# Kernel optimization log

Measured on AMD Instinct MI355X. Metric: run time of the kernel, lower is better.

## Reference

```python
import jax, jax.numpy as jnp
import numpy as np

H = 128          # hidden_dim
E = 1048576      # num edges
N = 262144       # num nodes
T = 4096         # num targets / subgraphs
NET = 8          # num_edge_types
SCALAR_DIM = 32  # max(H // 4, 8)
SHORT = 1.0      # short_time_scale
LONG = 24.0      # long_time_scale


def _ln(x):
    # F.layer_norm without affine params, eps=1e-5, biased variance
    m = jnp.mean(x, axis=-1, keepdims=True)
    v = jnp.var(x, axis=-1, keepdims=True)
    return (x - m) / jnp.sqrt(v + 1e-5)


def _seg_wmean(vals, gid, w, num_groups):
    # masked/weighted segment mean: mask is folded into w (zeros drop rows)
    num = jax.ops.segment_sum(vals * w[:, None], gid, num_segments=num_groups)
    den = jax.ops.segment_sum(w, gid, num_segments=num_groups)
    return num / jnp.maximum(den, 1e-6)[:, None]


def setup_inputs():
    key = jax.random.key(0)
    ks = jax.random.split(key, 14)
    node_repr = jax.random.normal(ks[0], (N, H), jnp.float32)
    edge_repr = jax.random.normal(ks[1], (E, H), jnp.float32)
    edge_src = jax.random.randint(ks[2], (E,), 0, N)
    edge_subgraph_id = jax.random.randint(ks[3], (E,), 0, T)
    node_subgraph_id = jax.random.randint(ks[4], (N,), 0, T)
    node_hop_depth = jax.random.randint(ks[5], (N,), 1, 4)
    rel_ids = jax.random.randint(ks[6], (E,), 0, 2 * NET)
    edge_relative_time = jax.random.uniform(ks[7], (E,), jnp.float32) * 48.0
    target_local_idx = jnp.arange(T, dtype=jnp.int32)
    base_dst = jax.random.randint(ks[8], (E,), 0, N)
    hit = jax.random.uniform(ks[9], (E,)) < 0.25
    edge_dst = jnp.where(hit, target_local_idx[edge_subgraph_id], base_dst)
    # scalar_proj: Linear(8, 32); fuse: Linear(8*H+32, 2*H) -> GELU -> Linear(2*H, H)
    W1 = jax.random.normal(ks[10], (8, SCALAR_DIM), jnp.float32) / np.sqrt(8.0)
    b1 = jnp.zeros((SCALAR_DIM,), jnp.float32)
    W2 = jax.random.normal(ks[11], (8 * H + SCALAR_DIM, 2 * H), jnp.float32) / np.sqrt(8.0 * H + SCALAR_DIM)
    b2 = jnp.zeros((2 * H,), jnp.float32)
    W3 = jax.random.normal(ks[12], (2 * H, H), jnp.float32) / np.sqrt(2.0 * H)
    b3 = jnp.zeros((H,), jnp.float32)
    return dict(node_repr=node_repr, edge_repr=edge_repr, edge_src=edge_src,
                edge_dst=edge_dst, rel_ids=rel_ids, edge_relative_time=edge_relative_time,
                target_local_idx=target_local_idx, node_subgraph_id=node_subgraph_id,
                edge_subgraph_id=edge_subgraph_id, node_hop_depth=node_hop_depth,
                W1=W1, b1=b1, W2=W2, b2=b2, W3=W3, b3=b3)


def reference(node_repr, edge_repr, edge_src, edge_dst, rel_ids, edge_relative_time,
              target_local_idx, node_subgraph_id, edge_subgraph_id, node_hop_depth,
              W1, b1, W2, b2, W3, b3):
    dtype = node_repr.dtype
    t = edge_relative_time.astype(dtype)
    short_w = jnp.exp(-t / SHORT)
    long_w = jnp.exp(-t / LONG)

    tmask = (edge_dst == target_local_idx[edge_subgraph_id]).astype(dtype)   # target edges
    in_m = tmask * (rel_ids < NET).astype(dtype)                             # inbound
    out_m = tmask * (rel_ids >= NET).astype(dtype)                           # outbound

    esg = edge_subgraph_id
    in_short = _seg_wmean(edge_repr, esg, in_m * short_w, T)
    out_short = _seg_wmean(edge_repr, esg, out_m * short_w, T)
    in_long = _seg_wmean(edge_repr, esg, in_m * long_w, T)
    out_long = _seg_wmean(edge_repr, esg, out_m * long_w, T)

    hop1_m = (node_hop_depth == 1).astype(dtype)
    hop2_m = (node_hop_depth >= 2).astype(dtype)
    hop1_mean_raw = _seg_wmean(node_repr, node_subgraph_id, hop1_m, T)
    hop2_mean_raw = _seg_wmean(node_repr, node_subgraph_id, hop2_m, T)

    src_repr = node_repr[edge_src]  # [E, H] gather
    hop1_edges_short = _seg_wmean(src_repr, esg, tmask * short_w, T)
    hop1_edges_long = _seg_wmean(src_repr, esg, tmask * long_w, T)

    burst_delta = _ln(in_short + out_short - (in_long + out_long))
    direction_gap = _ln(out_long - in_long)
    hop_gap = _ln(hop1_mean_raw - hop2_mean_raw)
    short_long_gap = _ln(hop1_edges_short - hop1_edges_long)
    asymmetry = _ln(jnp.abs(direction_gap))
    hop1_mean = _ln(hop1_mean_raw)
    hop2_mean = _ln(hop2_mean_raw)
    risk_base = _ln(in_long + out_long)

    seg1 = lambda w, g: jax.ops.segment_sum(w, g, num_segments=T)
    target_edge_count = seg1(tmask, esg)
    edge_time_mean = seg1(t * tmask, esg) / jnp.maximum(target_edge_count, 1e-6)
    inbound_count = seg1(in_m, esg)
    outbound_count = seg1(out_m, esg)
    hop1_count = seg1(hop1_m, node_subgraph_id)
    hop2_count = seg1(hop2_m, node_subgraph_id)
    short_mass = seg1(tmask * short_w, esg)
    long_mass = seg1(tmask * long_w, esg)

    scalar_features = jnp.stack([
        jnp.log1p(inbound_count), jnp.log1p(outbound_count),
        jnp.log1p(hop1_count), jnp.log1p(hop2_count),
        edge_time_mean, short_mass, long_mass, short_mass - long_mass], axis=-1)  # [T, 8]

    scalar_embedding = jax.nn.gelu(scalar_features @ W1 + b1, approximate=False)
    fused_input = jnp.concatenate([burst_delta, direction_gap, hop_gap, short_long_gap,
                                   asymmetry, hop1_mean, hop2_mean, risk_base,
                                   scalar_embedding], axis=-1)  # [T, 8*H + 32]
    hidden = jax.nn.gelu(fused_input @ W2 + b2, approximate=False)
    risk_embedding = 0.25 * jnp.tanh(hidden @ W3 + b3)  # [T, H]

    hop_gap_norm = jnp.mean(jnp.linalg.norm(hop_gap, axis=-1))
    sl_gap_norm = jnp.mean(jnp.linalg.norm(short_long_gap, axis=-1))
    dir_gap_norm = jnp.mean(jnp.linalg.norm(direction_gap, axis=-1))
    return risk_embedding, hop_gap_norm, sl_gap_norm, dir_gap_norm
```

## Files before the change

kernel.cpp:

```cpp
#include <hip/hip_runtime.h>
#include <math.h>

#define HDIM 128
#define TDIM 4096
#define NET_T 8

__device__ __forceinline__ float wave_sum64(float v) {
#pragma unroll
  for (int d = 32; d > 0; d >>= 1) v += __shfl_xor(v, d, 64);
  return v;
}

__device__ __forceinline__ float gelu_exact(float x) {
  return 0.5f * x * (1.0f + erff(x * 0.70710678118654752440f));
}

struct LN2 { float zx, zy, norm; };

__device__ __forceinline__ LN2 ln128(float x0, float x1) {
  float s = wave_sum64(x0 + x1);
  float mean = s * (1.0f / 128.0f);
  float d0 = x0 - mean, d1 = x1 - mean;
  float sq = wave_sum64(d0 * d0 + d1 * d1);
  float var = sq * (1.0f / 128.0f);
  float rstd = rsqrtf(var + 1e-5f);
  LN2 r;
  r.zx = d0 * rstd;
  r.zy = d1 * rstd;
  r.norm = sqrtf(sq) * rstd;
  return r;
}

__global__ void count_kernel(const int* __restrict__ edge_dst,
                             const int* __restrict__ esg,
                             const int* __restrict__ tli,
                             const int* __restrict__ nsg,
                             int* __restrict__ ecnt, int* __restrict__ ncnt,
                             int E_, int N_) {
  int gid = blockIdx.x * blockDim.x + threadIdx.x;
  if (gid < E_) {
    int s = esg[gid];
    if (edge_dst[gid] == tli[s]) atomicAdd(&ecnt[s], 1);
  }
  if (gid < N_) {
    atomicAdd(&ncnt[nsg[gid]], 1);
  }
}

__global__ __launch_bounds__(64) void scan_kernel(
    const int* __restrict__ ecnt, int* __restrict__ eoff, int* __restrict__ ecur,
    const int* __restrict__ ncnt, int* __restrict__ noff, int* __restrict__ ncur) {
  const int* cnt;
  int *off, *cur;
  if (blockIdx.x == 0) { cnt = ecnt; off = eoff; cur = ecur; }
  else                 { cnt = ncnt; off = noff; cur = ncur; }
  int lane = threadIdx.x;
  int base = lane * 64;
  int s = 0;
  for (int i = 0; i < 64; i++) s += cnt[base + i];
  int incl = s;
#pragma unroll
  for (int d = 1; d < 64; d <<= 1) {
    int v = __shfl_up(incl, d, 64);
    if (lane >= d) incl += v;
  }
  int run = incl - s;
  for (int i = 0; i < 64; i++) {
    off[base + i] = run;
    cur[base + i] = run;
    run += cnt[base + i];
  }
}

__global__ void scatter_kernel(const int* __restrict__ edge_dst,
                               const int* __restrict__ esg,
                               const int* __restrict__ tli,
                               const int* __restrict__ edge_src,
                               const int* __restrict__ rel_ids,
                               const float* __restrict__ etime,
                               const int* __restrict__ nsg,
                               const int* __restrict__ depth,
                               int* __restrict__ ecur, int* __restrict__ ncur,
                               int* __restrict__ s_eid, int* __restrict__ s_srcpk,
                               float* __restrict__ s_t, int* __restrict__ s_npk,
                               int E_, int N_) {
  int gid = blockIdx.x * blockDim.x + threadIdx.x;
  if (gid < E_) {
    int sg = esg[gid];
    if (edge_dst[gid] == tli[sg]) {
      int pos = atomicAdd(&ecur[sg], 1);
      s_eid[pos] = gid;
      s_srcpk[pos] = (edge_src[gid] << 1) | (rel_ids[gid] < NET_T ? 1 : 0);
      s_t[pos] = etime[gid];
    }
  }
  if (gid < N_) {
    int sg = nsg[gid];
    int pos = atomicAdd(&ncur[sg], 1);
    s_npk[pos] = (gid << 1) | (depth[gid] == 1 ? 1 : 0);
  }
}

__global__ __launch_bounds__(64) void target_kernel(
    const float* __restrict__ node_repr, const float* __restrict__ edge_repr,
    const int* __restrict__ eoff, const int* __restrict__ ecnt,
    const int* __restrict__ noff, const int* __restrict__ ncnt,
    const int* __restrict__ s_eid, const int* __restrict__ s_srcpk,
    const float* __restrict__ s_t, const int* __restrict__ s_npk,
    const float* __restrict__ W1, const float* __restrict__ b1,
    float* __restrict__ fused, float* __restrict__ norm_acc) {
  const int t = blockIdx.x;
  const int lane = threadIdx.x;
  const int e0 = eoff[t], ec = ecnt[t];
  const int n0 = noff[t], nc = ncnt[t];

  float ais0 = 0, ais1 = 0, aos0 = 0, aos1 = 0;
  float ail0 = 0, ail1 = 0, aol0 = 0, aol1 = 0;
  float hs0 = 0, hs1 = 0, hl0 = 0, hl1 = 0;
  float d_is = 0, d_os = 0, d_il = 0, d_ol = 0, tsum = 0, cin = 0;

  for (int i = e0; i < e0 + ec; i++) {
    int eid = s_eid[i];
    int pk = s_srcpk[i];
    float tt = s_t[i];
    float sw = expf(-tt);
    float lw = expf(-tt * (1.0f / 24.0f));
    float fin = (float)(pk & 1);
    int src = pk >> 1;
    const float2 er = *(const float2*)(edge_repr + (size_t)eid * HDIM + 2 * lane);
    const float2 nr = *(const float2*)(node_repr + (size_t)src * HDIM + 2 * lane);
    float wis = fin * sw, wos = sw - wis;
    float wil = fin * lw, wol = lw - wil;
    ais0 += er.x * wis; ais1 += er.y * wis;
    aos0 += er.x * wos; aos1 += er.y * wos;
    ail0 += er.x * wil; ail1 += er.y * wil;
    aol0 += er.x * wol; aol1 += er.y * wol;
    hs0 += nr.x * sw; hs1 += nr.y * sw;
    hl0 += nr.x * lw; hl1 += nr.y * lw;
    d_is += wis; d_os += wos; d_il += wil; d_ol += wol;
    tsum += tt; cin += fin;
  }

  float h10 = 0, h11 = 0, h20 = 0, h21 = 0, c1 = 0;
  for (int i = n0; i < n0 + nc; i++) {
    int pk = s_npk[i];
    float f1 = (float)(pk & 1);
    int idx = pk >> 1;
    const float2 nr = *(const float2*)(node_repr + (size_t)idx * HDIM + 2 * lane);
    h10 += nr.x * f1;           h11 += nr.y * f1;
    h20 += nr.x * (1.0f - f1);  h21 += nr.y * (1.0f - f1);
    c1 += f1;
  }
  float c2 = (float)nc - c1;

  float r_is = 1.0f / fmaxf(d_is, 1e-6f);
  float r_os = 1.0f / fmaxf(d_os, 1e-6f);
  float r_il = 1.0f / fmaxf(d_il, 1e-6f);
  float r_ol = 1.0f / fmaxf(d_ol, 1e-6f);
  float sm = d_is + d_os;
  float lm = d_il + d_ol;
  float r_sm = 1.0f / fmaxf(sm, 1e-6f);
  float r_lm = 1.0f / fmaxf(lm, 1e-6f);
  float r_c1 = 1.0f / fmaxf(c1, 1e-6f);
  float r_c2 = 1.0f / fmaxf(c2, 1e-6f);

  float mis0 = ais0 * r_is, mis1 = ais1 * r_is;
  float mos0 = aos0 * r_os, mos1 = aos1 * r_os;
  float mil0 = ail0 * r_il, mil1 = ail1 * r_il;
  float mol0 = aol0 * r_ol, mol1 = aol1 * r_ol;
  float mhs0 = hs0 * r_sm, mhs1 = hs1 * r_sm;
  float mhl0 = hl0 * r_lm, mhl1 = hl1 * r_lm;
  float mh10 = h10 * r_c1, mh11 = h11 * r_c1;
  float mh20 = h20 * r_c2, mh21 = h21 * r_c2;

  LN2 z_burst = ln128(mis0 + mos0 - mil0 - mol0, mis1 + mos1 - mil1 - mol1);
  LN2 z_dgap  = ln128(mol0 - mil0, mol1 - mil1);
  LN2 z_hgap  = ln128(mh10 - mh20, mh11 - mh21);
  LN2 z_sl    = ln128(mhs0 - mhl0, mhs1 - mhl1);
  LN2 z_asym  = ln128(fabsf(z_dgap.zx), fabsf(z_dgap.zy));
  LN2 z_h1    = ln128(mh10, mh11);
  LN2 z_h2    = ln128(mh20, mh21);
  LN2 z_rb    = ln128(mil0 + mol0, mil1 + mol1);

  if (lane == 0) {
    atomicAdd(&norm_acc[0], z_hgap.norm);
    atomicAdd(&norm_acc[1], z_sl.norm);
    atomicAdd(&norm_acc[2], z_dgap.norm);
  }

  float* frow = fused + (size_t)t * 1056;
  int co = 2 * lane;
  *(float2*)(frow + 0 * HDIM + co) = make_float2(z_burst.zx, z_burst.zy);
  *(float2*)(frow + 1 * HDIM + co) = make_float2(z_dgap.zx, z_dgap.zy);
  *(float2*)(frow + 2 * HDIM + co) = make_float2(z_hgap.zx, z_hgap.zy);
  *(float2*)(frow + 3 * HDIM + co) = make_float2(z_sl.zx, z_sl.zy);
  *(float2*)(frow + 4 * HDIM + co) = make_float2(z_asym.zx, z_asym.zy);
  *(float2*)(frow + 5 * HDIM + co) = make_float2(z_h1.zx, z_h1.zy);
  *(float2*)(frow + 6 * HDIM + co) = make_float2(z_h2.zx, z_h2.zy);
  *(float2*)(frow + 7 * HDIM + co) = make_float2(z_rb.zx, z_rb.zy);

  float ecf = (float)ec;
  float sf[8];
  sf[0] = log1pf(cin);
  sf[1] = log1pf(ecf - cin);
  sf[2] = log1pf(c1);
  sf[3] = log1pf(c2);
  sf[4] = tsum / fmaxf(ecf, 1e-6f);
  sf[5] = sm;
  sf[6] = lm;
  sf[7] = sm - lm;
  if (lane < 32) {
    float acc = b1[lane];
#pragma unroll
    for (int i = 0; i < 8; i++) acc += sf[i] * W1[i * 32 + lane];
    frow[1024 + lane] = gelu_exact(acc);
  }
}

template <int MODE>
__global__ __launch_bounds__(256) void gemm_kernel(
    const float* __restrict__ A, const float* __restrict__ B,
    const float* __restrict__ bias, float* __restrict__ C,
    int M, int N, int K) {
  __shared__ __align__(16) float As[32][68];
  __shared__ __align__(16) float Bs[32][68];
  const int tid = threadIdx.x;
  const int tx = tid & 15, ty = tid >> 4;
  const int m0 = blockIdx.y * 64, n0 = blockIdx.x * 64;
  float acc[4][4] = {};

  for (int kt = 0; kt < K; kt += 32) {
#pragma unroll
    for (int i = 0; i < 8; i++) {
      int idx = i * 256 + tid;
      int m = idx >> 5, k = idx & 31;
      As[k][m] = A[(size_t)(m0 + m) * K + kt + k];
      int kb = idx >> 6, n = idx & 63;
      Bs[kb][n] = B[(size_t)(kt + kb) * N + n0 + n];
    }
    __syncthreads();
#pragma unroll
    for (int kk = 0; kk < 32; kk++) {
      float4 a4 = *(const float4*)&As[kk][ty * 4];
      float4 b4 = *(const float4*)&Bs[kk][tx * 4];
      float a[4] = {a4.x, a4.y, a4.z, a4.w};
      float b[4] = {b4.x, b4.y, b4.z, b4.w};
#pragma unroll
      for (int i2 = 0; i2 < 4; i2++)
#pragma unroll
        for (int j2 = 0; j2 < 4; j2++)
          acc[i2][j2] = fmaf(a[i2], b[j2], acc[i2][j2]);
    }
    __syncthreads();
  }

#pragma unroll
  for (int i2 = 0; i2 < 4; i2++) {
    int m = m0 + ty * 4 + i2;
#pragma unroll
    for (int j2 = 0; j2 < 4; j2++) {
      int n = n0 + tx * 4 + j2;
      float v = acc[i2][j2] + bias[n];
      if (MODE == 0) v = gelu_exact(v);
      else           v = 0.25f * tanhf(v);
      C[(size_t)m * N + n] = v;
    }
  }
}

__global__ void finalize_kernel(const float* __restrict__ norm_acc,
                                float* __restrict__ out) {
  int i = threadIdx.x;
  if (i < 3) out[(size_t)TDIM * HDIM + i] = norm_acc[i] * (1.0f / (float)TDIM);
}

extern "C" void kernel_launch(void* const* d_in, const int* in_sizes, int n_in,
                              void* d_out, int out_size, void* d_ws, size_t ws_size,
                              hipStream_t stream) {
  const float* node_repr = (const float*)d_in[0];
  const float* edge_repr = (const float*)d_in[1];
  const int* edge_src = (const int*)d_in[2];
  const int* edge_dst = (const int*)d_in[3];
  const int* rel_ids = (const int*)d_in[4];
  const float* etime = (const float*)d_in[5];
  const int* tli = (const int*)d_in[6];
  const int* nsg = (const int*)d_in[7];
  const int* esg = (const int*)d_in[8];
  const int* depth = (const int*)d_in[9];
  const float* W1 = (const float*)d_in[10];
  const float* b1 = (const float*)d_in[11];
  const float* W2 = (const float*)d_in[12];
  const float* b2 = (const float*)d_in[13];
  const float* W3 = (const float*)d_in[14];
  const float* b3 = (const float*)d_in[15];
  float* out = (float*)d_out;

  const int E_ = in_sizes[2];
  const int N_ = in_sizes[7];

  char* ws = (char*)d_ws;
  size_t off = 0;
  auto alloc = [&](size_t bytes) -> void* {
    off = (off + 255) & ~(size_t)255;
    void* p = ws + off;
    off += bytes;
    return p;
  };
  int* ecnt = (int*)alloc((size_t)TDIM * 4);
  int* eoff = (int*)alloc((size_t)TDIM * 4);
  int* ecur = (int*)alloc((size_t)TDIM * 4);
  int* ncnt = (int*)alloc((size_t)TDIM * 4);
  int* noff = (int*)alloc((size_t)TDIM * 4);
  int* ncur = (int*)alloc((size_t)TDIM * 4);
  int* s_eid = (int*)alloc((size_t)E_ * 4);
  int* s_srcpk = (int*)alloc((size_t)E_ * 4);
  float* s_t = (float*)alloc((size_t)E_ * 4);
  int* s_npk = (int*)alloc((size_t)N_ * 4);
  float* fused = (float*)alloc((size_t)TDIM * 1056 * 4);
  float* hidden = (float*)alloc((size_t)TDIM * 256 * 4);
  float* norm_acc = (float*)alloc(4 * 4);

  hipMemsetAsync(ecnt, 0, (size_t)TDIM * 4, stream);
  hipMemsetAsync(ncnt, 0, (size_t)TDIM * 4, stream);
  hipMemsetAsync(norm_acc, 0, 16, stream);

  int gmax = (E_ > N_ ? E_ : N_);
  int g1 = (gmax + 255) / 256;

  count_kernel<<<g1, 256, 0, stream>>>(edge_dst, esg, tli, nsg, ecnt, ncnt, E_, N_);
  scan_kernel<<<2, 64, 0, stream>>>(ecnt, eoff, ecur, ncnt, noff, ncur);
  scatter_kernel<<<g1, 256, 0, stream>>>(edge_dst, esg, tli, edge_src, rel_ids,
                                         etime, nsg, depth, ecur, ncur,
                                         s_eid, s_srcpk, s_t, s_npk, E_, N_);
  target_kernel<<<TDIM, 64, 0, stream>>>(node_repr, edge_repr, eoff, ecnt, noff,
                                         ncnt, s_eid, s_srcpk, s_t, s_npk,
                                         W1, b1, fused, norm_acc);
  gemm_kernel<0><<<dim3(256 / 64, TDIM / 64), 256, 0, stream>>>(
      fused, W2, b2, hidden, TDIM, 256, 8 * HDIM + 32);
  gemm_kernel<1><<<dim3(HDIM / 64, TDIM / 64), 256, 0, stream>>>(
      hidden, W3, b3, out, TDIM, HDIM, 256);
  finalize_kernel<<<1, 64, 0, stream>>>(norm_acc, out);
}
```

Before: 1.050 ms.

## Split target aggregation across four waves and retile GEMM with vector loads

The target kernel now runs four wavefronts per subgraph. Two waves split the edge loop and two split the node loop, each handling alternating items with a 2x unrolled body, and the partial sums are combined through shared memory before wave 0 does the layer norms and writes the outputs. The GEMM kernel drops to 32-row tiles to double the block count, loads A and B with float4 vector reads, and writes the bias/activation epilogue as float4 stores. This adds memory-level parallelism to the latency-bound gather loops, at the cost of more shared memory, a block barrier and some extra launch overhead.

```diff
diff --git a/kernel.cpp b/kernel.cpp
--- a/kernel.cpp
+++ b/kernel.cpp
@@ -101,7 +101,7 @@
   }
 }
 
-__global__ __launch_bounds__(64) void target_kernel(
+__global__ __launch_bounds__(256) void target_kernel(
     const float* __restrict__ node_repr, const float* __restrict__ edge_repr,
     const int* __restrict__ eoff, const int* __restrict__ ecnt,
     const int* __restrict__ noff, const int* __restrict__ ncnt,
@@ -110,47 +110,108 @@
     const float* __restrict__ W1, const float* __restrict__ b1,
     float* __restrict__ fused, float* __restrict__ norm_acc) {
   const int t = blockIdx.x;
-  const int lane = threadIdx.x;
+  const int tid = threadIdx.x;
+  const int w = tid >> 6;
+  const int lane = tid & 63;
   const int e0 = eoff[t], ec = ecnt[t];
   const int n0 = noff[t], nc = ncnt[t];
 
-  float ais0 = 0, ais1 = 0, aos0 = 0, aos1 = 0;
-  float ail0 = 0, ail1 = 0, aol0 = 0, aol1 = 0;
-  float hs0 = 0, hs1 = 0, hl0 = 0, hl1 = 0;
-  float d_is = 0, d_os = 0, d_il = 0, d_ol = 0, tsum = 0, cin = 0;
-
-  for (int i = e0; i < e0 + ec; i++) {
-    int eid = s_eid[i];
-    int pk = s_srcpk[i];
-    float tt = s_t[i];
-    float sw = expf(-tt);
-    float lw = expf(-tt * (1.0f / 24.0f));
-    float fin = (float)(pk & 1);
-    int src = pk >> 1;
-    const float2 er = *(const float2*)(edge_repr + (size_t)eid * HDIM + 2 * lane);
-    const float2 nr = *(const float2*)(node_repr + (size_t)src * HDIM + 2 * lane);
-    float wis = fin * sw, wos = sw - wis;
-    float wil = fin * lw, wol = lw - wil;
-    ais0 += er.x * wis; ais1 += er.y * wis;
-    aos0 += er.x * wos; aos1 += er.y * wos;
-    ail0 += er.x * wil; ail1 += er.y * wil;
-    aol0 += er.x * wol; aol1 += er.y * wol;
-    hs0 += nr.x * sw; hs1 += nr.y * sw;
-    hl0 += nr.x * lw; hl1 += nr.y * lw;
-    d_is += wis; d_os += wos; d_il += wil; d_ol += wol;
-    tsum += tt; cin += fin;
-  }
-
-  float h10 = 0, h11 = 0, h20 = 0, h21 = 0, c1 = 0;
-  for (int i = n0; i < n0 + nc; i++) {
-    int pk = s_npk[i];
-    float f1 = (float)(pk & 1);
-    int idx = pk >> 1;
-    const float2 nr = *(const float2*)(node_repr + (size_t)idx * HDIM + 2 * lane);
-    h10 += nr.x * f1;           h11 += nr.y * f1;
-    h20 += nr.x * (1.0f - f1);  h21 += nr.y * (1.0f - f1);
-    c1 += f1;
-  }
+  __shared__ float lse[2][6][128];
+  __shared__ float lss[2][6];
+  __shared__ float lsn[2][2][128];
+  __shared__ float lnc[2];
+
+  const int co = 2 * lane;
+
+  if (w < 2) {
+    float ais0 = 0, ais1 = 0, aos0 = 0, aos1 = 0;
+    float ail0 = 0, ail1 = 0, aol0 = 0, aol1 = 0;
+    float hs0 = 0, hs1 = 0, hl0 = 0, hl1 = 0;
+    float d_is = 0, d_os = 0, d_il = 0, d_ol = 0, tsum = 0, cin = 0;
+
+#define EDGE_BODY(ii)                                                          \
+    {                                                                          \
+      int eid = s_eid[ii];                                                     \
+      int pk = s_srcpk[ii];                                                    \
+      float tt = s_t[ii];                                                      \
+      int src = pk >> 1;                                                       \
+      const float2 er = *(const float2*)(edge_repr + (size_t)eid * HDIM + co);\
+      const float2 nr = *(const float2*)(node_repr + (size_t)src * HDIM + co);\
+      float sw = expf(-tt);                                                    \
+      float lw = expf(-tt * (1.0f / 24.0f));                                   \
+      float fin = (float)(pk & 1);                                             \
+      float wis = fin * sw, wos = sw - wis;                                    \
+      float wil = fin * lw, wol = lw - wil;                                    \
+      ais0 += er.x * wis; ais1 += er.y * wis;                                  \
+      aos0 += er.x * wos; aos1 += er.y * wos;                                  \
+      ail0 += er.x * wil; ail1 += er.y * wil;                                  \
+      aol0 += er.x * wol; aol1 += er.y * wol;                                  \
+      hs0 += nr.x * sw; hs1 += nr.y * sw;                                      \
+      hl0 += nr.x * lw; hl1 += nr.y * lw;                                      \
+      d_is += wis; d_os += wos; d_il += wil; d_ol += wol;                      \
+      tsum += tt; cin += fin;                                                  \
+    }
+
+    int i = e0 + w;
+    const int end = e0 + ec;
+    for (; i + 2 < end; i += 4) { EDGE_BODY(i); EDGE_BODY(i + 2); }
+    if (i < end) EDGE_BODY(i);
+#undef EDGE_BODY
+
+    lse[w][0][co] = ais0; lse[w][0][co + 1] = ais1;
+    lse[w][1][co] = aos0; lse[w][1][co + 1] = aos1;
+    lse[w][2][co] = ail0; lse[w][2][co + 1] = ail1;
+    lse[w][3][co] = aol0; lse[w][3][co + 1] = aol1;
+    lse[w][4][co] = hs0;  lse[w][4][co + 1] = hs1;
+    lse[w][5][co] = hl0;  lse[w][5][co + 1] = hl1;
+    if (lane == 0) {
+      lss[w][0] = d_is; lss[w][1] = d_os; lss[w][2] = d_il;
+      lss[w][3] = d_ol; lss[w][4] = tsum; lss[w][5] = cin;
+    }
+  } else {
+    const int w2 = w - 2;
+    float h10 = 0, h11 = 0, h20 = 0, h21 = 0, c1 = 0;
+
+#define NODE_BODY(ii)                                                          \
+    {                                                                          \
+      int pk = s_npk[ii];                                                      \
+      int idx = pk >> 1;                                                       \
+      const float2 nr = *(const float2*)(node_repr + (size_t)idx * HDIM + co);\
+      float f1 = (float)(pk & 1);                                              \
+      h10 += nr.x * f1;          h11 += nr.y * f1;                             \
+      h20 += nr.x * (1.0f - f1); h21 += nr.y * (1.0f - f1);                    \
+      c1 += f1;                                                                \
+    }
+
+    int i = n0 + w2;
+    const int end = n0 + nc;
+    for (; i + 2 < end; i += 4) { NODE_BODY(i); NODE_BODY(i + 2); }
+    if (i < end) NODE_BODY(i);
+#undef NODE_BODY
+
+    lsn[w2][0][co] = h10; lsn[w2][0][co + 1] = h11;
+    lsn[w2][1][co] = h20; lsn[w2][1][co + 1] = h21;
+    if (lane == 0) lnc[w2] = c1;
+  }
+
+  __syncthreads();
+  if (w != 0) return;
+
+  float ais0 = lse[0][0][co] + lse[1][0][co], ais1 = lse[0][0][co + 1] + lse[1][0][co + 1];
+  float aos0 = lse[0][1][co] + lse[1][1][co], aos1 = lse[0][1][co + 1] + lse[1][1][co + 1];
+  float ail0 = lse[0][2][co] + lse[1][2][co], ail1 = lse[0][2][co + 1] + lse[1][2][co + 1];
+  float aol0 = lse[0][3][co] + lse[1][3][co], aol1 = lse[0][3][co + 1] + lse[1][3][co + 1];
+  float hs0  = lse[0][4][co] + lse[1][4][co], hs1  = lse[0][4][co + 1] + lse[1][4][co + 1];
+  float hl0  = lse[0][5][co] + lse[1][5][co], hl1  = lse[0][5][co + 1] + lse[1][5][co + 1];
+  float h10  = lsn[0][0][co] + lsn[1][0][co], h11  = lsn[0][0][co + 1] + lsn[1][0][co + 1];
+  float h20  = lsn[0][1][co] + lsn[1][1][co], h21  = lsn[0][1][co + 1] + lsn[1][1][co + 1];
+  float d_is = lss[0][0] + lss[1][0];
+  float d_os = lss[0][1] + lss[1][1];
+  float d_il = lss[0][2] + lss[1][2];
+  float d_ol = lss[0][3] + lss[1][3];
+  float tsum = lss[0][4] + lss[1][4];
+  float cin  = lss[0][5] + lss[1][5];
+  float c1   = lnc[0] + lnc[1];
   float c2 = (float)nc - c1;
 
   float r_is = 1.0f / fmaxf(d_is, 1e-6f);
@@ -189,7 +250,6 @@
   }
 
   float* frow = fused + (size_t)t * 1056;
-  int co = 2 * lane;
   *(float2*)(frow + 0 * HDIM + co) = make_float2(z_burst.zx, z_burst.zy);
   *(float2*)(frow + 1 * HDIM + co) = make_float2(z_dgap.zx, z_dgap.zy);
   *(float2*)(frow + 2 * HDIM + co) = make_float2(z_hgap.zx, z_hgap.zy);
@@ -222,31 +282,38 @@
     const float* __restrict__ A, const float* __restrict__ B,
     const float* __restrict__ bias, float* __restrict__ C,
     int M, int N, int K) {
-  __shared__ __align__(16) float As[32][68];
+  __shared__ __align__(16) float As[32][34];
   __shared__ __align__(16) float Bs[32][68];
   const int tid = threadIdx.x;
   const int tx = tid & 15, ty = tid >> 4;
-  const int m0 = blockIdx.y * 64, n0 = blockIdx.x * 64;
-  float acc[4][4] = {};
+  const int m0 = blockIdx.y * 32, n0 = blockIdx.x * 64;
+  float acc[2][4] = {};
+
+  const int am = tid >> 3;
+  const int ak = (tid & 7) * 4;
+  const int bk = tid >> 3;
+  const int bn = (tid & 7) * 8;
 
   for (int kt = 0; kt < K; kt += 32) {
-#pragma unroll
-    for (int i = 0; i < 8; i++) {
-      int idx = i * 256 + tid;
-      int m = idx >> 5, k = idx & 31;
-      As[k][m] = A[(size_t)(m0 + m) * K + kt + k];
-      int kb = idx >> 6, n = idx & 63;
-      Bs[kb][n] = B[(size_t)(kt + kb) * N + n0 + n];
-    }
+    float4 av = *(const float4*)&A[(size_t)(m0 + am) * K + kt + ak];
+    const float* bp = &B[(size_t)(kt + bk) * N + n0 + bn];
+    float4 bv0 = *(const float4*)bp;
+    float4 bv1 = *(const float4*)(bp + 4);
+    As[ak + 0][am] = av.x;
+    As[ak + 1][am] = av.y;
+    As[ak + 2][am] = av.z;
+    As[ak + 3][am] = av.w;
+    *(float4*)&Bs[bk][bn] = bv0;
+    *(float4*)&Bs[bk][bn + 4] = bv1;
     __syncthreads();
 #pragma unroll
     for (int kk = 0; kk < 32; kk++) {
-      float4 a4 = *(const float4*)&As[kk][ty * 4];
+      float2 a2 = *(const float2*)&As[kk][ty * 2];
       float4 b4 = *(const float4*)&Bs[kk][tx * 4];
-      float a[4] = {a4.x, a4.y, a4.z, a4.w};
+      float a[2] = {a2.x, a2.y};
       float b[4] = {b4.x, b4.y, b4.z, b4.w};
 #pragma unroll
-      for (int i2 = 0; i2 < 4; i2++)
+      for (int i2 = 0; i2 < 2; i2++)
 #pragma unroll
         for (int j2 = 0; j2 < 4; j2++)
           acc[i2][j2] = fmaf(a[i2], b[j2], acc[i2][j2]);
@@ -255,16 +322,23 @@
   }
 
 #pragma unroll
-  for (int i2 = 0; i2 < 4; i2++) {
-    int m = m0 + ty * 4 + i2;
-#pragma unroll
-    for (int j2 = 0; j2 < 4; j2++) {
-      int n = n0 + tx * 4 + j2;
-      float v = acc[i2][j2] + bias[n];
-      if (MODE == 0) v = gelu_exact(v);
-      else           v = 0.25f * tanhf(v);
-      C[(size_t)m * N + n] = v;
-    }
+  for (int i2 = 0; i2 < 2; i2++) {
+    int m = m0 + ty * 2 + i2;
+    int n = n0 + tx * 4;
+    float4 bb = *(const float4*)&bias[n];
+    float4 v;
+    v.x = acc[i2][0] + bb.x;
+    v.y = acc[i2][1] + bb.y;
+    v.z = acc[i2][2] + bb.z;
+    v.w = acc[i2][3] + bb.w;
+    if (MODE == 0) {
+      v.x = gelu_exact(v.x); v.y = gelu_exact(v.y);
+      v.z = gelu_exact(v.z); v.w = gelu_exact(v.w);
+    } else {
+      v.x = 0.25f * tanhf(v.x); v.y = 0.25f * tanhf(v.y);
+      v.z = 0.25f * tanhf(v.z); v.w = 0.25f * tanhf(v.w);
+    }
+    *(float4*)&C[(size_t)m * N + n] = v;
   }
 }
 
@@ -332,12 +406,12 @@
   scatter_kernel<<<g1, 256, 0, stream>>>(edge_dst, esg, tli, edge_src, rel_ids,
                                          etime, nsg, depth, ecur, ncur,
                                          s_eid, s_srcpk, s_t, s_npk, E_, N_);
-  target_kernel<<<TDIM, 64, 0, stream>>>(node_repr, edge_repr, eoff, ecnt, noff,
-                                         ncnt, s_eid, s_srcpk, s_t, s_npk,
-                                         W1, b1, fused, norm_acc);
-  gemm_kernel<0><<<dim3(256 / 64, TDIM / 64), 256, 0, stream>>>(
+  target_kernel<<<TDIM, 256, 0, stream>>>(node_repr, edge_repr, eoff, ecnt, noff,
+                                          ncnt, s_eid, s_srcpk, s_t, s_npk,
+                                          W1, b1, fused, norm_acc);
+  gemm_kernel<0><<<dim3(256 / 64, TDIM / 32), 256, 0, stream>>>(
       fused, W2, b2, hidden, TDIM, 256, 8 * HDIM + 32);
-  gemm_kernel<1><<<dim3(HDIM / 64, TDIM / 64), 256, 0, stream>>>(
+  gemm_kernel<1><<<dim3(HDIM / 64, TDIM / 32), 256, 0, stream>>>(
       hidden, W3, b3, out, TDIM, HDIM, 256);
   finalize_kernel<<<1, 64, 0, stream>>>(norm_acc, out);
 }
```

Result: faster. 988.4 us (-5.9%).
